# Kernel tuning notes

Measured on AMD Instinct MI355X. Metric: run time of the kernel, lower is better.

The kernel has to match this reference:

```python
import jax, jax.numpy as jnp
import numpy as np

N_HEAD = 16

def setup_inputs() -> dict:
    key = jax.random.key(0)
    ks = jax.random.split(key, 5)
    C = 1024
    s = 0.02
    return {
        "x": jax.random.normal(ks[0], (4, 2048, C), dtype=jnp.float32),
        "w_attn": jax.random.normal(ks[1], (C, 3 * C), dtype=jnp.float32) * s,
        "b_attn": jnp.zeros((3 * C,), dtype=jnp.float32),
        "w_proj": jax.random.normal(ks[2], (C, C), dtype=jnp.float32) * s,
        "b_proj": jnp.zeros((C,), dtype=jnp.float32),
    }

def reference(x, w_attn, b_attn, w_proj, b_proj):
    B, T, C = x.shape
    H = N_HEAD
    D = C // H
    qkv = x @ w_attn + b_attn                      # [B,T,3C]
    q, k, v = jnp.split(qkv, 3, axis=-1)
    # [B,H,T,D]
    q = q.reshape(B, T, H, D).transpose(0, 2, 1, 3)
    k = k.reshape(B, T, H, D).transpose(0, 2, 1, 3)
    v = v.reshape(B, T, H, D).transpose(0, 2, 1, 3)
    scale = 1.0 / np.sqrt(D).astype(np.float32)
    attn = jnp.einsum('bhtd,bhsd->bhts', q, k) * scale   # [B,H,T,T]
    causal = jnp.tril(jnp.ones((T, T), dtype=bool))
    attn = jnp.where(causal, attn, -jnp.inf)
    attn = jax.nn.softmax(attn, axis=-1)
    y = jnp.einsum('bhts,bhsd->bhtd', attn, v)           # [B,H,T,D]
    y = y.transpose(0, 2, 1, 3).reshape(B, T, C)
    return y @ w_proj + b_proj
```

## Files before the change

kernel.cpp:

```cpp
#include <hip/hip_runtime.h>
#include <hip/hip_bf16.h>

typedef short short8 __attribute__((ext_vector_type(8)));
typedef float f32x4 __attribute__((ext_vector_type(4)));

typedef __attribute__((address_space(1))) void as1_void;
typedef __attribute__((address_space(3))) void as3_void;

__device__ __forceinline__ unsigned short f2bf(float f) {
    __hip_bfloat16 h = __float2bfloat16(f);
    return __builtin_bit_cast(unsigned short, h);
}

__device__ __forceinline__ float exp2fast(float x) {
    return __builtin_amdgcn_exp2f(x);
}

__device__ __forceinline__ void gload16(const unsigned short* g, unsigned short* l) {
    __builtin_amdgcn_global_load_lds((as1_void*)g, (as3_void*)l, 16, 0, 0);
}

__global__ __launch_bounds__(256) void conv_f32_to_bf16(
    const float* __restrict__ in, unsigned short* __restrict__ out, int n4) {
    int i = blockIdx.x * 256 + threadIdx.x;
    if (i >= n4) return;
    float4 v = ((const float4*)in)[i];
    ushort4 o;
    o.x = f2bf(v.x); o.y = f2bf(v.y); o.z = f2bf(v.z); o.w = f2bf(v.w);
    ((ushort4*)out)[i] = o;
}

__global__ __launch_bounds__(256) void transpose_f32_to_bf16(
    const float* __restrict__ W, unsigned short* __restrict__ WT, int K, int N) {
    __shared__ float tile[32][33];
    int tx = threadIdx.x, ty = threadIdx.y;
    int n0 = blockIdx.x * 32, k0 = blockIdx.y * 32;
#pragma unroll
    for (int j = 0; j < 4; ++j)
        tile[ty + j * 8][tx] = W[(size_t)(k0 + ty + j * 8) * N + n0 + tx];
    __syncthreads();
#pragma unroll
    for (int j = 0; j < 4; ++j)
        WT[(size_t)(n0 + ty + j * 8) * K + k0 + tx] = f2bf(tile[tx][ty + j * 8]);
}

template <int MODE>
__global__ __launch_bounds__(256, 2) void gemm_bt(
    const unsigned short* __restrict__ A,
    const unsigned short* __restrict__ Bt,
    const float* __restrict__ bias,
    void* __restrict__ out0,
    unsigned short* __restrict__ out1,
    int M, int N, int K) {
    __shared__ unsigned short sA[128 * 32];
    __shared__ unsigned short sB[128 * 32];
    const int tid = threadIdx.x;
    const int lane = tid & 63;
    const int w = tid >> 6;
    const int wr = (w >> 1) * 64;
    const int wc = (w & 1) * 64;
    const size_t arow0 = (size_t)blockIdx.x * 128;
    const size_t brow0 = (size_t)blockIdx.y * 128;

    const int grow = (w << 5) + (lane >> 2);
    const int gcol = (lane & 3) << 3;
    const unsigned short* pA0 = A + (arow0 + grow) * (size_t)K + gcol;
    const unsigned short* pB0 = Bt + (brow0 + grow) * (size_t)K + gcol;
    unsigned short* lA = sA + (w << 10);
    unsigned short* lB = sB + (w << 10);

    f32x4 acc[4][4] = {};
    const int fr = lane & 15;
    const int fk = (lane >> 4) << 3;

    for (int k0 = 0; k0 < K; k0 += 32) {
        __syncthreads();
        gload16(pA0 + k0, lA);
        gload16(pA0 + 16 * (size_t)K + k0, lA + 512);
        gload16(pB0 + k0, lB);
        gload16(pB0 + 16 * (size_t)K + k0, lB + 512);
        __syncthreads();

        short8 af[4], bfr[4];
#pragma unroll
        for (int i = 0; i < 4; ++i)
            af[i] = *(const short8*)&sA[(wr + i * 16 + fr) * 32 + fk];
#pragma unroll
        for (int i = 0; i < 4; ++i)
            bfr[i] = *(const short8*)&sB[(wc + i * 16 + fr) * 32 + fk];
#pragma unroll
        for (int mi = 0; mi < 4; ++mi)
#pragma unroll
            for (int ni = 0; ni < 4; ++ni)
                acc[mi][ni] = __builtin_amdgcn_mfma_f32_16x16x32_bf16(
                    af[mi], bfr[ni], acc[mi][ni], 0, 0, 0);
    }

    const int fq = (lane >> 4) << 2;
    if constexpr (MODE == 0) {
#pragma unroll
        for (int mi = 0; mi < 4; ++mi)
#pragma unroll
            for (int ni = 0; ni < 4; ++ni) {
                size_t r = arow0 + wr + mi * 16 + fq;
                size_t c = brow0 + wc + ni * 16 + fr;
                float bv = bias[c];
#pragma unroll
                for (int j = 0; j < 4; ++j)
                    ((float*)out0)[(r + j) * (size_t)N + c] = acc[mi][ni][j] + bv;
            }
    } else {
        const bool isv = (int)(brow0 + wc) >= 2048;
        if (isv) {
#pragma unroll
            for (int mi = 0; mi < 4; ++mi)
#pragma unroll
                for (int ni = 0; ni < 4; ++ni) {
                    int c = (int)brow0 + wc + ni * 16 + fr;
                    float bv = bias[c];
                    int cv = c - 2048;
                    int r0 = (int)arow0 + wr + mi * 16 + fq;
                    int bb = r0 >> 11, t0 = r0 & 2047;
                    unsigned int lo = (unsigned int)f2bf(acc[mi][ni][0] + bv) |
                                      ((unsigned int)f2bf(acc[mi][ni][1] + bv) << 16);
                    unsigned int hi = (unsigned int)f2bf(acc[mi][ni][2] + bv) |
                                      ((unsigned int)f2bf(acc[mi][ni][3] + bv) << 16);
                    *(uint2*)&out1[(((size_t)(bb * 1024 + cv)) << 11) + t0] =
                        make_uint2(lo, hi);
                }
        } else {
            const float qs = ((int)(brow0 + wc) < 1024) ? 0.125f * 1.4426950408889634f
                                                        : 1.0f;
#pragma unroll
            for (int mi = 0; mi < 4; ++mi)
#pragma unroll
                for (int ni = 0; ni < 4; ++ni) {
                    size_t r = arow0 + wr + mi * 16 + fq;
                    size_t c = brow0 + wc + ni * 16 + fr;
                    float bv = bias[c];
#pragma unroll
                    for (int j = 0; j < 4; ++j)
                        ((unsigned short*)out0)[(r + j) * 2048 + c] =
                            f2bf((acc[mi][ni][j] + bv) * qs);
                }
        }
    }
}

__global__ __launch_bounds__(256, 2) void attn_mfma(
    const unsigned short* __restrict__ qk,
    const unsigned short* __restrict__ vt,
    unsigned short* __restrict__ y,
    int BH) {
    constexpr int T = 2048;
    constexpr float THR = 8.0f;

    __shared__ __align__(16) unsigned short sK[64 * 64];
    __shared__ __align__(16) unsigned short sV[64 * 64];
    __shared__ __align__(16) unsigned short sP[4][32 * 64];

    const int tid = threadIdx.x;
    const int lane = tid & 63;
    const int w = tid >> 6;
    const int l15 = lane & 15;
    const int g = lane >> 4;

    const int bh = blockIdx.x % BH;
    const int p = blockIdx.x / BH;
    const int b = bh >> 4;
    const int h = bh & 15;

    const unsigned short* kbase = qk + ((size_t)(b * T)) * 2048 + 1024 + h * 64;
    const unsigned short* vbase = vt + ((size_t)(b * 1024 + h * 64)) * 2048;
    unsigned short* sPw = sP[w];

    const int srow = tid >> 3;
    const int c16 = tid & 7;
    const int swz = ((c16 ^ (srow & 7)) << 3);

    short8 vones;
#pragma unroll
    for (int i = 0; i < 8; ++i) vones[i] = (short)0x3F80;

    for (int half = 0; half < 2; ++half) {
        const int qt = half ? p : (15 - p);
        const int q0 = qt << 7;
        const int qw0 = q0 + w * 32;

        short8 aq[2][2];
        {
            const unsigned short* qbase =
                qk + ((size_t)(b * T + qw0)) * 2048 + h * 64;
#pragma unroll
            for (int mi = 0; mi < 2; ++mi)
#pragma unroll
                for (int kc = 0; kc < 2; ++kc)
                    aq[mi][kc] = *(const short8*)(qbase +
                                                  (size_t)(mi * 16 + l15) * 2048 +
                                                  g * 8 + kc * 32);
        }

        f32x4 O[2][4] = {};
        float m_st[2][4], l_st[2][4];
#pragma unroll
        for (int mi = 0; mi < 2; ++mi)
#pragma unroll
            for (int r = 0; r < 4; ++r) { m_st[mi][r] = -1e30f; l_st[mi][r] = 0.f; }

        const int nt = (q0 + 128) >> 6;

        uint4 kd0, kd1, vd0, vd1;
        __syncthreads();
        kd0 = *(const uint4*)(kbase + (size_t)(srow) * 2048 + c16 * 8);
        kd1 = *(const uint4*)(kbase + (size_t)(srow + 32) * 2048 + c16 * 8);
        vd0 = *(const uint4*)(vbase + (size_t)srow * 2048 + c16 * 8);
        vd1 = *(const uint4*)(vbase + (size_t)(srow + 32) * 2048 + c16 * 8);
        *(uint4*)&sK[srow * 64 + swz] = kd0;
        *(uint4*)&sK[(srow + 32) * 64 + swz] = kd1;
        *(uint4*)&sV[srow * 64 + swz] = vd0;
        *(uint4*)&sV[(srow + 32) * 64 + swz] = vd1;
        __syncthreads();

        for (int it = 0; it < nt; ++it) {
            const int s0 = it << 6;
            const bool haveNext = (it + 1 < nt);
            if (haveNext) {
                const int s1 = s0 + 64;
                kd0 = *(const uint4*)(kbase + (size_t)(s1 + srow) * 2048 + c16 * 8);
                kd1 = *(const uint4*)(kbase + (size_t)(s1 + srow + 32) * 2048 + c16 * 8);
                vd0 = *(const uint4*)(vbase + (size_t)srow * 2048 + s1 + c16 * 8);
                vd1 = *(const uint4*)(vbase + (size_t)(srow + 32) * 2048 + s1 + c16 * 8);
            }

            if (s0 <= qw0 + 31) {
                f32x4 sacc[2][4] = {};
                {
                    short8 bk[4][2];
#pragma unroll
                    for (int ni = 0; ni < 4; ++ni) {
                        const int row = ni * 16 + l15;
#pragma unroll
                        for (int kc = 0; kc < 2; ++kc)
                            bk[ni][kc] = *(const short8*)&sK[row * 64 +
                                                             (((g + kc * 4) ^ (row & 7))
                                                              << 3)];
                    }
                    __builtin_amdgcn_s_setprio(1);
#pragma unroll
                    for (int kc = 0; kc < 2; ++kc)
#pragma unroll
                        for (int mi = 0; mi < 2; ++mi)
#pragma unroll
                            for (int ni = 0; ni < 4; ++ni)
                                sacc[mi][ni] = __builtin_amdgcn_mfma_f32_16x16x32_bf16(
                                    aq[mi][kc], bk[ni][kc], sacc[mi][ni], 0, 0, 0);
                    __builtin_amdgcn_s_setprio(0);
                }

                const bool needMask = (s0 + 63 > qw0);
                float mxl[2][4];
                bool big = false;
#pragma unroll
                for (int mi = 0; mi < 2; ++mi) {
#pragma unroll
                    for (int reg = 0; reg < 4; ++reg) {
                        if (needMask) {
                            const int qg = qw0 + mi * 16 + g * 4 + reg;
#pragma unroll
                            for (int ni = 0; ni < 4; ++ni) {
                                float v = sacc[mi][ni][reg];
                                sacc[mi][ni][reg] =
                                    (s0 + ni * 16 + l15 <= qg) ? v : -INFINITY;
                            }
                        }
                        float mx = fmaxf(fmaxf(sacc[mi][0][reg], sacc[mi][1][reg]),
                                         fmaxf(sacc[mi][2][reg], sacc[mi][3][reg]));
                        mxl[mi][reg] = mx;
                        big = big || (mx > m_st[mi][reg] + THR);
                    }
                }

                const bool resc = __any(big);
                float f_sc[2][4];
                if (resc) {
#pragma unroll
                    for (int mi = 0; mi < 2; ++mi) {
#pragma unroll
                        for (int reg = 0; reg < 4; ++reg) {
                            float mx = mxl[mi][reg];
                            mx = fmaxf(mx, __shfl_xor(mx, 1));
                            mx = fmaxf(mx, __shfl_xor(mx, 2));
                            mx = fmaxf(mx, __shfl_xor(mx, 4));
                            mx = fmaxf(mx, __shfl_xor(mx, 8));
                            const float mn = fmaxf(m_st[mi][reg], mx);
                            f_sc[mi][reg] = exp2fast(m_st[mi][reg] - mn);
                            m_st[mi][reg] = mn;
                        }
                    }
#pragma unroll
                    for (int mi = 0; mi < 2; ++mi)
#pragma unroll
                        for (int di = 0; di < 4; ++di)
#pragma unroll
                            for (int reg = 0; reg < 4; ++reg)
                                O[mi][di][reg] *= f_sc[mi][reg];
                }

#pragma unroll
                for (int mi = 0; mi < 2; ++mi) {
#pragma unroll
                    for (int reg = 0; reg < 4; ++reg) {
                        const int q_loc = mi * 16 + g * 4 + reg;
                        const float mrow = m_st[mi][reg];
#pragma unroll
                        for (int ni = 0; ni < 4; ++ni) {
                            float pv = exp2fast(sacc[mi][ni][reg] - mrow);
                            const int s = ni * 16 + l15;
                            sPw[q_loc * 64 +
                                ((((s >> 3) ^ (q_loc & 7)) << 3) | (s & 7))] = f2bf(pv);
                        }
                    }
                }

                short8 aP[2][2], bv[4][2];
#pragma unroll
                for (int mi = 0; mi < 2; ++mi) {
                    const int row = mi * 16 + l15;
#pragma unroll
                    for (int kc = 0; kc < 2; ++kc)
                        aP[mi][kc] = *(const short8*)&sPw[row * 64 +
                                                          (((g + kc * 4) ^ (row & 7))
                                                           << 3)];
                }
#pragma unroll
                for (int di = 0; di < 4; ++di) {
                    const int row = di * 16 + l15;
#pragma unroll
                    for (int kc = 0; kc < 2; ++kc)
                        bv[di][kc] = *(const short8*)&sV[row * 64 +
                                                         (((g + kc * 4) ^ (row & 7))
                                                          << 3)];
                }
                f32x4 lacc[2] = {};
                __builtin_amdgcn_s_setprio(1);
#pragma unroll
                for (int kc = 0; kc < 2; ++kc)
#pragma unroll
                    for (int mi = 0; mi < 2; ++mi)
                        lacc[mi] = __builtin_amdgcn_mfma_f32_16x16x32_bf16(
                            aP[mi][kc], vones, lacc[mi], 0, 0, 0);
#pragma unroll
                for (int kc = 0; kc < 2; ++kc)
#pragma unroll
                    for (int mi = 0; mi < 2; ++mi)
#pragma unroll
                        for (int di = 0; di < 4; ++di)
                            O[mi][di] = __builtin_amdgcn_mfma_f32_16x16x32_bf16(
                                aP[mi][kc], bv[di][kc], O[mi][di], 0, 0, 0);
                __builtin_amdgcn_s_setprio(0);
                if (resc) {
#pragma unroll
                    for (int mi = 0; mi < 2; ++mi)
#pragma unroll
                        for (int reg = 0; reg < 4; ++reg)
                            l_st[mi][reg] =
                                l_st[mi][reg] * f_sc[mi][reg] + lacc[mi][reg];
                } else {
#pragma unroll
                    for (int mi = 0; mi < 2; ++mi)
#pragma unroll
                        for (int reg = 0; reg < 4; ++reg)
                            l_st[mi][reg] += lacc[mi][reg];
                }
            }

            __syncthreads();
            if (haveNext) {
                *(uint4*)&sK[srow * 64 + swz] = kd0;
                *(uint4*)&sK[(srow + 32) * 64 + swz] = kd1;
                *(uint4*)&sV[srow * 64 + swz] = vd0;
                *(uint4*)&sV[(srow + 32) * 64 + swz] = vd1;
                __syncthreads();
            }
        }

#pragma unroll
        for (int mi = 0; mi < 2; ++mi) {
#pragma unroll
            for (int reg = 0; reg < 4; ++reg) {
                const float inv = 1.0f / l_st[mi][reg];
                const int q = qw0 + mi * 16 + g * 4 + reg;
                const size_t base = (size_t)(b * T + q) * 1024 + h * 64 + l15;
#pragma unroll
                for (int di = 0; di < 4; ++di)
                    y[base + di * 16] = f2bf(O[mi][di][reg] * inv);
            }
        }
    }
}

extern "C" void kernel_launch(void* const* d_in, const int* in_sizes, int n_in,
                              void* d_out, int out_size, void* d_ws, size_t ws_size,
                              hipStream_t stream) {
    const float* x      = (const float*)d_in[0];
    const float* w_attn = (const float*)d_in[1];
    const float* b_attn = (const float*)d_in[2];
    const float* w_proj = (const float*)d_in[3];
    const float* b_proj = (const float*)d_in[4];

    const int C = 1024, T = 2048, H = 16;
    const int B = in_sizes[0] / (T * C);
    const int M = B * T;

    unsigned short* xb  = (unsigned short*)d_ws;
    unsigned short* wTa = xb + (size_t)M * C;
    unsigned short* wTp = wTa + (size_t)3 * C * C;
    unsigned short* qkb = wTp + (size_t)C * C;
    unsigned short* vtb = qkb + (size_t)M * 2 * C;
    unsigned short* y   = xb;

    int n4 = (M * C) / 4;
    conv_f32_to_bf16<<<(n4 + 255) / 256, 256, 0, stream>>>(x, xb, n4);
    transpose_f32_to_bf16<<<dim3(3 * C / 32, C / 32), dim3(32, 8), 0, stream>>>(
        w_attn, wTa, C, 3 * C);
    transpose_f32_to_bf16<<<dim3(C / 32, C / 32), dim3(32, 8), 0, stream>>>(
        w_proj, wTp, C, C);
    gemm_bt<2><<<dim3(M / 128, (3 * C) / 128), 256, 0, stream>>>(
        xb, wTa, b_attn, (void*)qkb, vtb, M, 3 * C, C);
    attn_mfma<<<dim3((B * H) * 8), 256, 0, stream>>>(qkb, vtb, y, B * H);
    gemm_bt<0><<<dim3(M / 128, C / 128), 256, 0, stream>>>(
        y, wTp, b_proj, d_out, nullptr, M, C, C);
}
```

Measured before the change: 188.9 us.

## Fuse x fp32-to-bf16 conversion into QKV GEMM and widen attention key tiles

Removes the standalone x conversion kernel. The QKV GEMM now loads fp32 x directly, converts it to bf16 in registers and stores it to LDS, which saves a full write and re-read of the bf16 copy of x. Separately, the attention kernel now processes 128 keys per iteration instead of 64, with a doubled K buffer, two V halves and a wider P buffer. That halves the loop trips and barriers, at the cost of more LDS and registers and more wasted work on masked diagonal tiles. The A-operand path in the QKV GEMM now goes through registers instead of direct global-to-LDS loads, which may add latency.

Result: slower. 230.0 us (+21.8%).

```diff
diff --git a/kernel.cpp b/kernel.cpp
--- a/kernel.cpp
+++ b/kernel.cpp
@@ -11,6 +11,9 @@
     __hip_bfloat16 h = __float2bfloat16(f);
     return __builtin_bit_cast(unsigned short, h);
 }
+__device__ __forceinline__ unsigned int pack2(float a, float b) {
+    return (unsigned int)f2bf(a) | ((unsigned int)f2bf(b) << 16);
+}
 
 __device__ __forceinline__ float exp2fast(float x) {
     return __builtin_amdgcn_exp2f(x);
@@ -18,16 +21,6 @@
 
 __device__ __forceinline__ void gload16(const unsigned short* g, unsigned short* l) {
     __builtin_amdgcn_global_load_lds((as1_void*)g, (as3_void*)l, 16, 0, 0);
-}
-
-__global__ __launch_bounds__(256) void conv_f32_to_bf16(
-    const float* __restrict__ in, unsigned short* __restrict__ out, int n4) {
-    int i = blockIdx.x * 256 + threadIdx.x;
-    if (i >= n4) return;
-    float4 v = ((const float4*)in)[i];
-    ushort4 o;
-    o.x = f2bf(v.x); o.y = f2bf(v.y); o.z = f2bf(v.z); o.w = f2bf(v.w);
-    ((ushort4*)out)[i] = o;
 }
 
 __global__ __launch_bounds__(256) void transpose_f32_to_bf16(
@@ -46,7 +39,7 @@
 
 template <int MODE>
 __global__ __launch_bounds__(256, 2) void gemm_bt(
-    const unsigned short* __restrict__ A,
+    const void* __restrict__ A,
     const unsigned short* __restrict__ Bt,
     const float* __restrict__ bias,
     void* __restrict__ out0,
@@ -64,7 +57,9 @@
 
     const int grow = (w << 5) + (lane >> 2);
     const int gcol = (lane & 3) << 3;
-    const unsigned short* pA0 = A + (arow0 + grow) * (size_t)K + gcol;
+    const unsigned short* pA0 =
+        (const unsigned short*)A + (arow0 + grow) * (size_t)K + gcol;
+    const float* pAf = (const float*)A + (arow0 + grow) * (size_t)K + gcol;
     const unsigned short* pB0 = Bt + (brow0 + grow) * (size_t)K + gcol;
     unsigned short* lA = sA + (w << 10);
     unsigned short* lB = sB + (w << 10);
@@ -75,10 +70,25 @@
 
     for (int k0 = 0; k0 < K; k0 += 32) {
         __syncthreads();
-        gload16(pA0 + k0, lA);
-        gload16(pA0 + 16 * (size_t)K + k0, lA + 512);
-        gload16(pB0 + k0, lB);
-        gload16(pB0 + 16 * (size_t)K + k0, lB + 512);
+        if constexpr (MODE == 0) {
+            gload16(pA0 + k0, lA);
+            gload16(pA0 + 16 * (size_t)K + k0, lA + 512);
+            gload16(pB0 + k0, lB);
+            gload16(pB0 + 16 * (size_t)K + k0, lB + 512);
+        } else {
+            float4 xa0 = *(const float4*)(pAf + k0);
+            float4 xa1 = *(const float4*)(pAf + k0 + 4);
+            float4 xb0 = *(const float4*)(pAf + 16 * (size_t)K + k0);
+            float4 xb1 = *(const float4*)(pAf + 16 * (size_t)K + k0 + 4);
+            gload16(pB0 + k0, lB);
+            gload16(pB0 + 16 * (size_t)K + k0, lB + 512);
+            uint4 w0 = make_uint4(pack2(xa0.x, xa0.y), pack2(xa0.z, xa0.w),
+                                  pack2(xa1.x, xa1.y), pack2(xa1.z, xa1.w));
+            uint4 w1 = make_uint4(pack2(xb0.x, xb0.y), pack2(xb0.z, xb0.w),
+                                  pack2(xb1.x, xb1.y), pack2(xb1.z, xb1.w));
+            *(uint4*)&sA[grow * 32 + gcol] = w0;
+            *(uint4*)&sA[(grow + 16) * 32 + gcol] = w1;
+        }
         __syncthreads();
 
         short8 af[4], bfr[4];
@@ -121,10 +131,8 @@
                     int cv = c - 2048;
                     int r0 = (int)arow0 + wr + mi * 16 + fq;
                     int bb = r0 >> 11, t0 = r0 & 2047;
-                    unsigned int lo = (unsigned int)f2bf(acc[mi][ni][0] + bv) |
-                                      ((unsigned int)f2bf(acc[mi][ni][1] + bv) << 16);
-                    unsigned int hi = (unsigned int)f2bf(acc[mi][ni][2] + bv) |
-                                      ((unsigned int)f2bf(acc[mi][ni][3] + bv) << 16);
+                    unsigned int lo = pack2(acc[mi][ni][0] + bv, acc[mi][ni][1] + bv);
+                    unsigned int hi = pack2(acc[mi][ni][2] + bv, acc[mi][ni][3] + bv);
                     *(uint2*)&out1[(((size_t)(bb * 1024 + cv)) << 11) + t0] =
                         make_uint2(lo, hi);
                 }
@@ -155,9 +163,10 @@
     constexpr int T = 2048;
     constexpr float THR = 8.0f;
 
-    __shared__ __align__(16) unsigned short sK[64 * 64];
-    __shared__ __align__(16) unsigned short sV[64 * 64];
-    __shared__ __align__(16) unsigned short sP[4][32 * 64];
+    __shared__ __align__(16) unsigned short sK[128 * 64];
+    __shared__ __align__(16) unsigned short sVa[64 * 64];
+    __shared__ __align__(16) unsigned short sVb[64 * 64];
+    __shared__ __align__(16) unsigned short sP[4][32 * 128];
 
     const int tid = threadIdx.x;
     const int lane = tid & 63;
@@ -207,57 +216,68 @@
 #pragma unroll
             for (int r = 0; r < 4; ++r) { m_st[mi][r] = -1e30f; l_st[mi][r] = 0.f; }
 
-        const int nt = (q0 + 128) >> 6;
-
-        uint4 kd0, kd1, vd0, vd1;
+        const int nt = qt + 1;
+
+        uint4 kd[4], vd[4];
         __syncthreads();
-        kd0 = *(const uint4*)(kbase + (size_t)(srow) * 2048 + c16 * 8);
-        kd1 = *(const uint4*)(kbase + (size_t)(srow + 32) * 2048 + c16 * 8);
-        vd0 = *(const uint4*)(vbase + (size_t)srow * 2048 + c16 * 8);
-        vd1 = *(const uint4*)(vbase + (size_t)(srow + 32) * 2048 + c16 * 8);
-        *(uint4*)&sK[srow * 64 + swz] = kd0;
-        *(uint4*)&sK[(srow + 32) * 64 + swz] = kd1;
-        *(uint4*)&sV[srow * 64 + swz] = vd0;
-        *(uint4*)&sV[(srow + 32) * 64 + swz] = vd1;
+#pragma unroll
+        for (int rep = 0; rep < 4; ++rep)
+            kd[rep] = *(const uint4*)(kbase + (size_t)(srow + rep * 32) * 2048 +
+                                      c16 * 8);
+        vd[0] = *(const uint4*)(vbase + (size_t)srow * 2048 + c16 * 8);
+        vd[1] = *(const uint4*)(vbase + (size_t)(srow + 32) * 2048 + c16 * 8);
+        vd[2] = *(const uint4*)(vbase + (size_t)srow * 2048 + 64 + c16 * 8);
+        vd[3] = *(const uint4*)(vbase + (size_t)(srow + 32) * 2048 + 64 + c16 * 8);
+#pragma unroll
+        for (int rep = 0; rep < 4; ++rep)
+            *(uint4*)&sK[(srow + rep * 32) * 64 + swz] = kd[rep];
+        *(uint4*)&sVa[srow * 64 + swz] = vd[0];
+        *(uint4*)&sVa[(srow + 32) * 64 + swz] = vd[1];
+        *(uint4*)&sVb[srow * 64 + swz] = vd[2];
+        *(uint4*)&sVb[(srow + 32) * 64 + swz] = vd[3];
         __syncthreads();
 
         for (int it = 0; it < nt; ++it) {
-            const int s0 = it << 6;
+            const int s0 = it << 7;
             const bool haveNext = (it + 1 < nt);
             if (haveNext) {
-                const int s1 = s0 + 64;
-                kd0 = *(const uint4*)(kbase + (size_t)(s1 + srow) * 2048 + c16 * 8);
-                kd1 = *(const uint4*)(kbase + (size_t)(s1 + srow + 32) * 2048 + c16 * 8);
-                vd0 = *(const uint4*)(vbase + (size_t)srow * 2048 + s1 + c16 * 8);
-                vd1 = *(const uint4*)(vbase + (size_t)(srow + 32) * 2048 + s1 + c16 * 8);
+                const int s1 = s0 + 128;
+#pragma unroll
+                for (int rep = 0; rep < 4; ++rep)
+                    kd[rep] = *(const uint4*)(kbase +
+                                              (size_t)(s1 + srow + rep * 32) * 2048 +
+                                              c16 * 8);
+                vd[0] = *(const uint4*)(vbase + (size_t)srow * 2048 + s1 + c16 * 8);
+                vd[1] = *(const uint4*)(vbase + (size_t)(srow + 32) * 2048 + s1 +
+                                        c16 * 8);
+                vd[2] = *(const uint4*)(vbase + (size_t)srow * 2048 + s1 + 64 +
+                                        c16 * 8);
+                vd[3] = *(const uint4*)(vbase + (size_t)(srow + 32) * 2048 + s1 + 64 +
+                                        c16 * 8);
             }
 
             if (s0 <= qw0 + 31) {
-                f32x4 sacc[2][4] = {};
-                {
-                    short8 bk[4][2];
-#pragma unroll
-                    for (int ni = 0; ni < 4; ++ni) {
-                        const int row = ni * 16 + l15;
-#pragma unroll
-                        for (int kc = 0; kc < 2; ++kc)
-                            bk[ni][kc] = *(const short8*)&sK[row * 64 +
-                                                             (((g + kc * 4) ^ (row & 7))
-                                                              << 3)];
-                    }
-                    __builtin_amdgcn_s_setprio(1);
-#pragma unroll
-                    for (int kc = 0; kc < 2; ++kc)
-#pragma unroll
-                        for (int mi = 0; mi < 2; ++mi)
-#pragma unroll
-                            for (int ni = 0; ni < 4; ++ni)
-                                sacc[mi][ni] = __builtin_amdgcn_mfma_f32_16x16x32_bf16(
-                                    aq[mi][kc], bk[ni][kc], sacc[mi][ni], 0, 0, 0);
-                    __builtin_amdgcn_s_setprio(0);
-                }
-
-                const bool needMask = (s0 + 63 > qw0);
+                f32x4 sacc[2][8] = {};
+                __builtin_amdgcn_s_setprio(1);
+#pragma unroll
+                for (int ni = 0; ni < 8; ++ni) {
+                    const int row = ni * 16 + l15;
+                    short8 bk0 = *(const short8*)&sK[row * 64 +
+                                                     ((g ^ (row & 7)) << 3)];
+                    short8 bk1 = *(const short8*)&sK[row * 64 +
+                                                     (((g + 4) ^ (row & 7)) << 3)];
+                    sacc[0][ni] = __builtin_amdgcn_mfma_f32_16x16x32_bf16(
+                        aq[0][0], bk0, sacc[0][ni], 0, 0, 0);
+                    sacc[1][ni] = __builtin_amdgcn_mfma_f32_16x16x32_bf16(
+                        aq[1][0], bk0, sacc[1][ni], 0, 0, 0);
+                    sacc[0][ni] = __builtin_amdgcn_mfma_f32_16x16x32_bf16(
+                        aq[0][1], bk1, sacc[0][ni], 0, 0, 0);
+                    sacc[1][ni] = __builtin_amdgcn_mfma_f32_16x16x32_bf16(
+                        aq[1][1], bk1, sacc[1][ni], 0, 0, 0);
+                }
+                __builtin_amdgcn_s_setprio(0);
+
+                const bool needMask = (s0 + 127 > qw0);
                 float mxl[2][4];
                 bool big = false;
 #pragma unroll
@@ -267,14 +287,16 @@
                         if (needMask) {
                             const int qg = qw0 + mi * 16 + g * 4 + reg;
 #pragma unroll
-                            for (int ni = 0; ni < 4; ++ni) {
+                            for (int ni = 0; ni < 8; ++ni) {
                                 float v = sacc[mi][ni][reg];
                                 sacc[mi][ni][reg] =
                                     (s0 + ni * 16 + l15 <= qg) ? v : -INFINITY;
                             }
                         }
-                        float mx = fmaxf(fmaxf(sacc[mi][0][reg], sacc[mi][1][reg]),
-                                         fmaxf(sacc[mi][2][reg], sacc[mi][3][reg]));
+                        float mx = sacc[mi][0][reg];
+#pragma unroll
+                        for (int ni = 1; ni < 8; ++ni)
+                            mx = fmaxf(mx, sacc[mi][ni][reg]);
                         mxl[mi][reg] = mx;
                         big = big || (mx > m_st[mi][reg] + THR);
                     }
@@ -313,50 +335,41 @@
                         const int q_loc = mi * 16 + g * 4 + reg;
                         const float mrow = m_st[mi][reg];
 #pragma unroll
-                        for (int ni = 0; ni < 4; ++ni) {
+                        for (int ni = 0; ni < 8; ++ni) {
                             float pv = exp2fast(sacc[mi][ni][reg] - mrow);
                             const int s = ni * 16 + l15;
-                            sPw[q_loc * 64 +
+                            sPw[q_loc * 128 +
                                 ((((s >> 3) ^ (q_loc & 7)) << 3) | (s & 7))] = f2bf(pv);
                         }
                     }
                 }
 
-                short8 aP[2][2], bv[4][2];
-#pragma unroll
-                for (int mi = 0; mi < 2; ++mi) {
-                    const int row = mi * 16 + l15;
-#pragma unroll
-                    for (int kc = 0; kc < 2; ++kc)
-                        aP[mi][kc] = *(const short8*)&sPw[row * 64 +
-                                                          (((g + kc * 4) ^ (row & 7))
-                                                           << 3)];
-                }
-#pragma unroll
-                for (int di = 0; di < 4; ++di) {
-                    const int row = di * 16 + l15;
-#pragma unroll
-                    for (int kc = 0; kc < 2; ++kc)
-                        bv[di][kc] = *(const short8*)&sV[row * 64 +
-                                                         (((g + kc * 4) ^ (row & 7))
-                                                          << 3)];
-                }
                 f32x4 lacc[2] = {};
                 __builtin_amdgcn_s_setprio(1);
 #pragma unroll
-                for (int kc = 0; kc < 2; ++kc)
-#pragma unroll
-                    for (int mi = 0; mi < 2; ++mi)
-                        lacc[mi] = __builtin_amdgcn_mfma_f32_16x16x32_bf16(
-                            aP[mi][kc], vones, lacc[mi], 0, 0, 0);
-#pragma unroll
-                for (int kc = 0; kc < 2; ++kc)
-#pragma unroll
-                    for (int mi = 0; mi < 2; ++mi)
-#pragma unroll
-                        for (int di = 0; di < 4; ++di)
-                            O[mi][di] = __builtin_amdgcn_mfma_f32_16x16x32_bf16(
-                                aP[mi][kc], bv[di][kc], O[mi][di], 0, 0, 0);
+                for (int kc = 0; kc < 4; ++kc) {
+                    const unsigned short* sVh = (kc < 2) ? sVa : sVb;
+                    const int gg = g + (kc & 1) * 4;
+                    const int ch = g + kc * 4;
+                    short8 aP0 = *(const short8*)&sPw[l15 * 128 +
+                                                      ((ch ^ (l15 & 7)) << 3)];
+                    short8 aP1 = *(const short8*)&sPw[(16 + l15) * 128 +
+                                                      ((ch ^ (l15 & 7)) << 3)];
+                    lacc[0] = __builtin_amdgcn_mfma_f32_16x16x32_bf16(
+                        aP0, vones, lacc[0], 0, 0, 0);
+                    lacc[1] = __builtin_amdgcn_mfma_f32_16x16x32_bf16(
+                        aP1, vones, lacc[1], 0, 0, 0);
+#pragma unroll
+                    for (int di = 0; di < 4; ++di) {
+                        const int row = di * 16 + l15;
+                        short8 bv = *(const short8*)&sVh[row * 64 +
+                                                         ((gg ^ (row & 7)) << 3)];
+                        O[0][di] = __builtin_amdgcn_mfma_f32_16x16x32_bf16(
+                            aP0, bv, O[0][di], 0, 0, 0);
+                        O[1][di] = __builtin_amdgcn_mfma_f32_16x16x32_bf16(
+                            aP1, bv, O[1][di], 0, 0, 0);
+                    }
+                }
                 __builtin_amdgcn_s_setprio(0);
                 if (resc) {
 #pragma unroll
@@ -376,10 +389,13 @@
 
             __syncthreads();
             if (haveNext) {
-                *(uint4*)&sK[srow * 64 + swz] = kd0;
-                *(uint4*)&sK[(srow + 32) * 64 + swz] = kd1;
-                *(uint4*)&sV[srow * 64 + swz] = vd0;
-                *(uint4*)&sV[(srow + 32) * 64 + swz] = vd1;
+#pragma unroll
+                for (int rep = 0; rep < 4; ++rep)
+                    *(uint4*)&sK[(srow + rep * 32) * 64 + swz] = kd[rep];
+                *(uint4*)&sVa[srow * 64 + swz] = vd[0];
+                *(uint4*)&sVa[(srow + 32) * 64 + swz] = vd[1];
+                *(uint4*)&sVb[srow * 64 + swz] = vd[2];
+                *(uint4*)&sVb[(srow + 32) * 64 + swz] = vd[3];
                 __syncthreads();
             }
         }
@@ -412,22 +428,19 @@
     const int B = in_sizes[0] / (T * C);
     const int M = B * T;
 
-    unsigned short* xb  = (unsigned short*)d_ws;
-    unsigned short* wTa = xb + (size_t)M * C;
+    unsigned short* yb  = (unsigned short*)d_ws;
+    unsigned short* wTa = yb + (size_t)M * C;
     unsigned short* wTp = wTa + (size_t)3 * C * C;
     unsigned short* qkb = wTp + (size_t)C * C;
     unsigned short* vtb = qkb + (size_t)M * 2 * C;
-    unsigned short* y   = xb;
-
-    int n4 = (M * C) / 4;
-    conv_f32_to_bf16<<<(n4 + 255) / 256, 256, 0, stream>>>(x, xb, n4);
+
     transpose_f32_to_bf16<<<dim3(3 * C / 32, C / 32), dim3(32, 8), 0, stream>>>(
         w_attn, wTa, C, 3 * C);
     transpose_f32_to_bf16<<<dim3(C / 32, C / 32), dim3(32, 8), 0, stream>>>(
         w_proj, wTp, C, C);
     gemm_bt<2><<<dim3(M / 128, (3 * C) / 128), 256, 0, stream>>>(
-        xb, wTa, b_attn, (void*)qkb, vtb, M, 3 * C, C);
-    attn_mfma<<<dim3((B * H) * 8), 256, 0, stream>>>(qkb, vtb, y, B * H);
+        (const void*)x, wTa, b_attn, (void*)qkb, vtb, M, 3 * C, C);
+    attn_mfma<<<dim3((B * H) * 8), 256, 0, stream>>>(qkb, vtb, yb, B * H);
     gemm_bt<0><<<dim3(M / 128, C / 128), 256, 0, stream>>>(
-        y, wTp, b_proj, d_out, nullptr, M, C, C);
-}
+        (const void*)yb, wTp, b_proj, d_out, nullptr, M, C, C);
+}
```
